# Optimization experiments

Measured on AMD Instinct MI355X. Metric: run time of the kernel, lower is better.

## Reference

```python
import jax, jax.numpy as jnp
import numpy as np

N, E, H, D_IN, L, G, T = 50000, 800000, 64, 64, 4, 128, 1

def _w(key, shape, fan_in):
    return jax.random.normal(key, shape, dtype=jnp.float32) / np.sqrt(fan_in)

def setup_inputs() -> dict:
    key = jax.random.key(0)
    ks = jax.random.split(key, 24)
    inp = {
        'x': jax.random.normal(ks[0], (N, D_IN), dtype=jnp.float32),
        'w': jax.random.normal(ks[1], (E, 1), dtype=jnp.float32),
        'src': jax.random.randint(ks[2], (E,), 0, N, dtype=jnp.int32),
        'dst': jax.random.randint(ks[3], (E,), 0, N, dtype=jnp.int32),
        'graph_id': jnp.sort(jax.random.randint(ks[4], (N,), 0, G, dtype=jnp.int32)),
        # input MLP (1 layer, last_activation None; SiLU applied in input_node_func)
        'W_in': _w(ks[5], (D_IN, H), D_IN), 'b_in': jnp.zeros((H,), jnp.float32),
        # per-layer message MLP: (2H+1 -> H -> H), SiLU mid and last
        'msg_W1': _w(ks[6], (L, 2 * H + 1, H), 2 * H + 1), 'msg_b1': jnp.zeros((L, H), jnp.float32),
        'msg_W2': _w(ks[7], (L, H, H), H), 'msg_b2': jnp.zeros((L, H), jnp.float32),
        # per-layer update MLP: (H -> H -> H), SiLU mid, last None
        'upd_W1': _w(ks[8], (L, H, H), H), 'upd_b1': jnp.zeros((L, H), jnp.float32),
        'upd_W2': _w(ks[9], (L, H, H), H), 'upd_b2': jnp.zeros((L, H), jnp.float32),
        # node-wise output MLP: (H -> H -> H), SiLU mid, last None
        'out_W1': _w(ks[10], (H, H), H), 'out_b1': jnp.zeros((H,), jnp.float32),
        'out_W2': _w(ks[11], (H, H), H), 'out_b2': jnp.zeros((H,), jnp.float32),
        # readout MLP: (3H -> H -> T), SiLU mid, last None
        'ro_W1': _w(ks[12], (3 * H, H), 3 * H), 'ro_b1': jnp.zeros((H,), jnp.float32),
        'ro_W2': _w(ks[13], (H, T), H), 'ro_b2': jnp.zeros((T,), jnp.float32),
    }
    return inp

def reference(x, w, src, dst, graph_id, W_in, b_in, msg_W1, msg_b1, msg_W2, msg_b2,
              upd_W1, upd_b1, upd_W2, upd_b2, out_W1, out_b1, out_W2, out_b2,
              ro_W1, ro_b1, ro_W2, ro_b2):
    silu = jax.nn.silu
    f = silu(x @ W_in + b_in)                                   # [N, H]
    sq = w * w                                                  # [E, 1]
    for l in range(L):
        mi = jnp.concatenate([f[src], f[dst], sq], axis=-1)     # [E, 2H+1]
        msg = silu(silu(mi @ msg_W1[l] + msg_b1[l]) @ msg_W2[l] + msg_b2[l])
        m = msg * jax.nn.sigmoid(msg)                           # gated message
        m_sum = jax.ops.segment_sum(m, dst, num_segments=N)     # scatter-sum to dst
        h_new = silu((m_sum + f) @ upd_W1[l] + upd_b1[l]) @ upd_W2[l] + upd_b2[l]
        f = h_new + f                                           # residual
    f = silu(f @ out_W1 + out_b1) @ out_W2 + out_b2             # node-wise output
    g_sum = jax.ops.segment_sum(f, graph_id, num_segments=G)
    cnt = jax.ops.segment_sum(jnp.ones((N, 1), f.dtype), graph_id, num_segments=G)
    g_mean = g_sum / jnp.maximum(cnt, 1.0)
    g_max = jax.ops.segment_max(f, graph_id, num_segments=G)
    readout = jnp.concatenate([g_sum, g_mean, g_max], axis=-1)  # [G, 3H]
    return silu(readout @ ro_W1 + ro_b1) @ ro_W2 + ro_b2        # [G, T]
```

## Files before the change

kernel.cpp:

```cpp
#include <hip/hip_runtime.h>

#define NN 50000
#define EE 800000
#define GG 128
#define LL 4
#define SCAN_B 196

typedef __bf16 bf16x8 __attribute__((ext_vector_type(8)));
typedef __bf16 bf16x4 __attribute__((ext_vector_type(4)));
typedef float  f32x4  __attribute__((ext_vector_type(4)));

__device__ __forceinline__ float silu_f(float x){
    float t = __builtin_amdgcn_exp2f(-1.44269504f * x);
    return x * __builtin_amdgcn_rcpf(1.0f + t);
}
__device__ __forceinline__ unsigned fenc(float v){
    unsigned u = __float_as_uint(v);
    return (u & 0x80000000u) ? ~u : (u | 0x80000000u);
}
__device__ __forceinline__ float fdec(unsigned u){
    return (u & 0x80000000u) ? __uint_as_float(u & 0x7fffffffu) : __uint_as_float(~u);
}

__global__ __launch_bounds__(256) void pack_k(
        const float* __restrict__ msgW1, const float* __restrict__ msgW2,
        const float* __restrict__ updW1, const float* __restrict__ updW2,
        const float* __restrict__ outW1, const float* __restrict__ outW2,
        const float* __restrict__ W_in, __bf16* __restrict__ pk){
    int m = blockIdx.x;
    const float* src;
    if(m<20){
        int l=m/5, r=m%5;
        if(r==0)      src = msgW1 + (size_t)l*129*64;
        else if(r==1) src = msgW1 + (size_t)l*129*64 + 64*64;
        else if(r==2) src = msgW2 + (size_t)l*64*64;
        else if(r==3) src = updW1 + (size_t)l*64*64;
        else          src = updW2 + (size_t)l*64*64;
    } else if(m==20) src=outW1; else if(m==21) src=outW2; else src=W_in;
    __bf16* dst = pk + (size_t)m*4096;
    int tid=threadIdx.x;
    #pragma unroll
    for(int i=0;i<16;++i){
        int idx = tid*16+i;
        int frag = idx>>9, lane=(idx>>3)&63, j=idx&7;
        int s=frag>>2, ng=frag&3, q=lane>>4, nn=lane&15;
        dst[idx] = (__bf16)src[(32*s+8*q+j)*64 + 16*ng + nn];
    }
}
__device__ __forceinline__ bf16x8 ldfrag(const __bf16* pk, int s, int ng, int lane){
    return *(const bf16x8*)&pk[(((s*4+ng)*64 + lane))*8];
}

__global__ __launch_bounds__(256) void input_mfma(const float* __restrict__ x,
        const __bf16* __restrict__ pkW, const float* __restrict__ bg,
        float* __restrict__ f, __bf16* __restrict__ f16, int N){
    int tid=threadIdx.x, wid=tid>>6, lane=tid&63;
    int q=lane>>4, nn=lane&15;
    bf16x8 Bf[2][4];
    #pragma unroll
    for(int s=0;s<2;++s)
        #pragma unroll
        for(int ng=0;ng<4;++ng) Bf[s][ng]=ldfrag(pkW,s,ng,lane);
    float bias[4];
    #pragma unroll
    for(int ng=0;ng<4;++ng) bias[ng]=bg[16*ng+nn];

    int ntiles=(N+15)/16;
    int gw=gridDim.x*4;
    for(int t=blockIdx.x*4+wid; t<ntiles; t+=gw){
        int m=t*16+nn; int mc=(m<N)?m:(N-1);
        float4 a0=*(const float4*)&x[(size_t)mc*64 + 8*q];
        float4 a1=*(const float4*)&x[(size_t)mc*64 + 8*q + 4];
        float4 a2=*(const float4*)&x[(size_t)mc*64 + 32 + 8*q];
        float4 a3=*(const float4*)&x[(size_t)mc*64 + 32 + 8*q + 4];
        bf16x8 af0, af1;
        af0[0]=(__bf16)a0.x; af0[1]=(__bf16)a0.y; af0[2]=(__bf16)a0.z; af0[3]=(__bf16)a0.w;
        af0[4]=(__bf16)a1.x; af0[5]=(__bf16)a1.y; af0[6]=(__bf16)a1.z; af0[7]=(__bf16)a1.w;
        af1[0]=(__bf16)a2.x; af1[1]=(__bf16)a2.y; af1[2]=(__bf16)a2.z; af1[3]=(__bf16)a2.w;
        af1[4]=(__bf16)a3.x; af1[5]=(__bf16)a3.y; af1[6]=(__bf16)a3.z; af1[7]=(__bf16)a3.w;
        #pragma unroll
        for(int ng=0;ng<4;++ng){
            f32x4 acc; acc[0]=bias[ng]; acc[1]=bias[ng]; acc[2]=bias[ng]; acc[3]=bias[ng];
            acc=__builtin_amdgcn_mfma_f32_16x16x32_bf16(af0,Bf[0][ng],acc,0,0,0);
            acc=__builtin_amdgcn_mfma_f32_16x16x32_bf16(af1,Bf[1][ng],acc,0,0,0);
            #pragma unroll
            for(int r=0;r<4;++r){
                int row=t*16+4*q+r;
                if(row<N){
                    float o=silu_f(acc[r]);
                    f[(size_t)row*64+16*ng+nn]=o;
                    f16[(size_t)row*64+16*ng+nn]=(__bf16)o;
                }
            }
        }
    }
}

__global__ void hist_k(const int* __restrict__ dst, int* __restrict__ deg, int E){
    int e=blockIdx.x*blockDim.x+threadIdx.x;
    if(e<E) atomicAdd(&deg[dst[e]],1);
}

__global__ __launch_bounds__(256) void scan1_k(const int* __restrict__ deg, int* __restrict__ curs,
        int* __restrict__ bsum, int N){
    __shared__ int sv[256];
    int tid=threadIdx.x;
    int idx=blockIdx.x*256+tid;
    int v=(idx<N)?deg[idx]:0;
    sv[tid]=v; __syncthreads();
    #pragma unroll
    for(int off=1; off<256; off<<=1){
        int a=(tid>=off)?sv[tid-off]:0;
        __syncthreads(); sv[tid]+=a; __syncthreads();
    }
    if(idx<N) curs[idx]=sv[tid]-v;
    if(tid==255) bsum[blockIdx.x]=sv[255];
}
__global__ __launch_bounds__(256) void scan2_k(int* __restrict__ bsum, int B){
    __shared__ int sv[256];
    int tid=threadIdx.x;
    int v=(tid<B)?bsum[tid]:0;
    sv[tid]=v; __syncthreads();
    #pragma unroll
    for(int off=1; off<256; off<<=1){
        int a=(tid>=off)?sv[tid-off]:0;
        __syncthreads(); sv[tid]+=a; __syncthreads();
    }
    if(tid<B) bsum[tid]=sv[tid]-v;
}
__global__ __launch_bounds__(256) void scan3_k(int* __restrict__ curs, const int* __restrict__ bsum, int N){
    int idx=blockIdx.x*256+threadIdx.x;
    if(idx<N) curs[idx]+=bsum[blockIdx.x];
}

__global__ void fill_k(const int* __restrict__ src, const int* __restrict__ dst,
                       const float* __restrict__ w, int* __restrict__ cursor,
                       int4* __restrict__ meta, int E){
    int e=blockIdx.x*blockDim.x+threadIdx.x;
    if(e<E){
        int d=dst[e];
        int r=atomicAdd(&cursor[d],1);
        float ww=w[e];
        int4 v; v.x=src[e]; v.y=d; v.z=__float_as_int(ww*ww); v.w=0;
        meta[r]=v;
    }
}

__global__ __launch_bounds__(256) void xy_mfma(const __bf16* __restrict__ f16,
        const __bf16* __restrict__ pkA, const __bf16* __restrict__ pkB,
        const float* __restrict__ b1, __bf16* __restrict__ XY,
        float* __restrict__ msum, int N){
    int tid=threadIdx.x, wid=tid>>6, lane=tid&63;
    int q=lane>>4, nn=lane&15;
    bf16x8 Bf[2][8];
    #pragma unroll
    for(int s=0;s<2;++s){
        #pragma unroll
        for(int ng=0;ng<4;++ng){ Bf[s][ng]=ldfrag(pkA,s,ng,lane); Bf[s][4+ng]=ldfrag(pkB,s,ng,lane); }
    }
    float bias[8];
    #pragma unroll
    for(int ng=0;ng<8;++ng) bias[ng]=(ng<4)?0.f:b1[16*(ng-4)+nn];
    int ntiles=(N+15)/16;
    int gw=gridDim.x*4;
    for(int t=blockIdx.x*4+wid; t<ntiles; t+=gw){
        int row=t*16+nn; if(row>=N) row=N-1;
        bf16x8 a0=*(const bf16x8*)&f16[(size_t)row*64 + 8*q];
        bf16x8 a1=*(const bf16x8*)&f16[(size_t)row*64 + 32 + 8*q];
        {
            float4 z; z.x=0.f; z.y=0.f; z.z=0.f; z.w=0.f;
            float4* mz=(float4*)(msum + (size_t)t*1024);
            int lim=(t*16+16<=N)?4:0;
            if(lim){
                #pragma unroll
                for(int i=0;i<4;++i) mz[i*64+lane]=z;
            } else {
                for(int rr=t*16; rr<N; ++rr) msum[(size_t)rr*64+lane]=0.f;
            }
        }
        #pragma unroll
        for(int ng=0;ng<8;++ng){
            f32x4 acc; acc[0]=bias[ng]; acc[1]=bias[ng]; acc[2]=bias[ng]; acc[3]=bias[ng];
            acc=__builtin_amdgcn_mfma_f32_16x16x32_bf16(a0,Bf[0][ng],acc,0,0,0);
            acc=__builtin_amdgcn_mfma_f32_16x16x32_bf16(a1,Bf[1][ng],acc,0,0,0);
            #pragma unroll
            for(int r=0;r<4;++r){
                int orow=t*16+4*q+r;
                if(orow<N) XY[(size_t)orow*128 + 16*ng + nn]=(__bf16)acc[r];
            }
        }
    }
}

__global__ __launch_bounds__(256) void edge_mfma4(
        const __bf16* __restrict__ XY, const int4* __restrict__ meta,
        const __bf16* __restrict__ pkW2,
        const float* __restrict__ W1, const float* __restrict__ b2,
        float* __restrict__ msum, int E){
    int tid=threadIdx.x, wid=tid>>6, lane=tid&63;
    int q=lane>>4, nn=lane&15;

    bf16x8 B2f[2][4];
    #pragma unroll
    for(int s=0;s<2;++s)
        #pragma unroll
        for(int ng=0;ng<4;++ng) B2f[s][ng]=ldfrag(pkW2,s,ng,lane);
    float w128lo[8], w128hi[8];
    #pragma unroll
    for(int j=0;j<8;++j){
        w128lo[j]=W1[128*64 + 8*q+j];
        w128hi[j]=W1[128*64 + 32+8*q+j];
    }
    float bias2[4];
    #pragma unroll
    for(int ng=0;ng<4;++ng) bias2[ng]=b2[16*ng+nn];

    __shared__ __align__(16) __bf16 sm16[4][32][68];
    int cpos = 4*(lane&15) + (lane>>4);

    int ntiles=E/32;
    int nw=gridDim.x*4;
    int chunk=(ntiles+nw-1)/nw;
    int wgl=blockIdx.x*4+wid;
    int t0=wgl*chunk, t1=t0+chunk; if(t1>ntiles) t1=ntiles;
    if(t0>=t1) return;

    int4 mv = meta[(size_t)t0*32 + (lane&31)];
    bf16x8 gx0lo,gx0hi,gy0lo,gy0hi,gx1lo,gx1hi,gy1lo,gy1hi;
    {
        int se0=__shfl(mv.x, nn,64),    de0=__shfl(mv.y, nn,64);
        int se1=__shfl(mv.x, 16+nn,64), de1=__shfl(mv.y, 16+nn,64);
        const __bf16* xp0=XY+(size_t)se0*128; const __bf16* yp0=XY+(size_t)de0*128+64;
        const __bf16* xp1=XY+(size_t)se1*128; const __bf16* yp1=XY+(size_t)de1*128+64;
        gx0lo=*(const bf16x8*)(xp0+8*q); gx0hi=*(const bf16x8*)(xp0+32+8*q);
        gy0lo=*(const bf16x8*)(yp0+8*q); gy0hi=*(const bf16x8*)(yp0+32+8*q);
        gx1lo=*(const bf16x8*)(xp1+8*q); gx1hi=*(const bf16x8*)(xp1+32+8*q);
        gy1lo=*(const bf16x8*)(yp1+8*q); gy1hi=*(const bf16x8*)(yp1+32+8*q);
    }
    int cur=__builtin_amdgcn_readlane(mv.y, 0);
    float vsum=0.f;

    for(int t=t0;t<t1;++t){
        bool hasn = (t+1<t1);
        int4 mvn = mv;
        if(hasn) mvn = meta[(size_t)(t+1)*32 + (lane&31)];

        int d_ = mv.y;
        float w2v = __int_as_float(mv.z);

        bf16x8 A0lo,A0hi,A1lo,A1hi;
        {
            float w2a = __shfl(w2v, nn, 64);
            float w2b = __shfl(w2v, 16+nn, 64);
            #pragma unroll
            for(int j=0;j<8;++j){
                A0lo[j]=(__bf16)silu_f((float)gx0lo[j] + (float)gy0lo[j] + w2a*w128lo[j]);
                A0hi[j]=(__bf16)silu_f((float)gx0hi[j] + (float)gy0hi[j] + w2a*w128hi[j]);
                A1lo[j]=(__bf16)silu_f((float)gx1lo[j] + (float)gy1lo[j] + w2b*w128lo[j]);
                A1hi[j]=(__bf16)silu_f((float)gx1hi[j] + (float)gy1hi[j] + w2b*w128hi[j]);
            }
        }
        if(hasn){
            int se0=__shfl(mvn.x, nn,64),    de0=__shfl(mvn.y, nn,64);
            int se1=__shfl(mvn.x, 16+nn,64), de1=__shfl(mvn.y, 16+nn,64);
            const __bf16* xp0=XY+(size_t)se0*128; const __bf16* yp0=XY+(size_t)de0*128+64;
            const __bf16* xp1=XY+(size_t)se1*128; const __bf16* yp1=XY+(size_t)de1*128+64;
            gx0lo=*(const bf16x8*)(xp0+8*q); gx0hi=*(const bf16x8*)(xp0+32+8*q);
            gy0lo=*(const bf16x8*)(yp0+8*q); gy0hi=*(const bf16x8*)(yp0+32+8*q);
            gx1lo=*(const bf16x8*)(xp1+8*q); gx1hi=*(const bf16x8*)(xp1+32+8*q);
            gy1lo=*(const bf16x8*)(yp1+8*q); gy1hi=*(const bf16x8*)(yp1+32+8*q);
        }
        #pragma unroll
        for(int h=0;h<2;++h){
            bf16x8 alo = h ? A1lo : A0lo;
            bf16x8 ahi = h ? A1hi : A0hi;
            f32x4 acc2[4];
            #pragma unroll
            for(int ng=0;ng<4;++ng){ f32x4 c; c[0]=bias2[ng]; c[1]=bias2[ng]; c[2]=bias2[ng]; c[3]=bias2[ng]; acc2[ng]=c; }
            #pragma unroll
            for(int ng=0;ng<4;++ng){
                acc2[ng]=__builtin_amdgcn_mfma_f32_16x16x32_bf16(alo,B2f[0][ng],acc2[ng],0,0,0);
                acc2[ng]=__builtin_amdgcn_mfma_f32_16x16x32_bf16(ahi,B2f[1][ng],acc2[ng],0,0,0);
            }
            #pragma unroll
            for(int r=0;r<4;++r){
                bf16x4 pv;
                #pragma unroll
                for(int ng=0;ng<4;++ng) pv[ng]=(__bf16)silu_f(silu_f(acc2[ng][r]));
                *(bf16x4*)&sm16[wid][16*h+4*q+r][4*nn] = pv;
            }
        }
        asm volatile("" ::: "memory");
        #pragma unroll
        for(int r=0;r<32;++r){
            int dr=__builtin_amdgcn_readlane(d_, r);
            if(dr!=cur){
                atomicAdd(&msum[(size_t)cur*64+lane], vsum);
                vsum=0.f; cur=dr;
            }
            vsum+=(float)sm16[wid][r][cpos];
        }
        asm volatile("" ::: "memory");
        mv = mvn;
    }
    atomicAdd(&msum[(size_t)cur*64+lane], vsum);
}

__global__ __launch_bounds__(256) void node_mfma(const float* __restrict__ A, const float* __restrict__ F,
        const __bf16* __restrict__ pkW1, const float* __restrict__ b1,
        const __bf16* __restrict__ pkW2, const float* __restrict__ b2,
        float* __restrict__ out, __bf16* __restrict__ out16, int N){
    int tid=threadIdx.x, wid=tid>>6, lane=tid&63;
    int q=lane>>4, nn=lane&15;

    bf16x8 B1f[2][4], B2f[2][4];
    #pragma unroll
    for(int s=0;s<2;++s)
        #pragma unroll
        for(int ng=0;ng<4;++ng){ B1f[s][ng]=ldfrag(pkW1,s,ng,lane); B2f[s][ng]=ldfrag(pkW2,s,ng,lane); }
    float bias1[4], bias2[4];
    #pragma unroll
    for(int ng=0;ng<4;++ng){ bias1[ng]=b1[16*ng+nn]; bias2[ng]=b2[16*ng+nn]; }

    __shared__ __align__(16) __bf16 sh1[4][16][72];
    __shared__ __align__(16) float sF[4][16][68];
    bool hasF = (F != nullptr);

    int ntiles=(N+15)/16;
    int gw=gridDim.x*4;
    for(int t=blockIdx.x*4+wid; t<ntiles; t+=gw){
        int m=t*16+nn;
        int mc=(m<N)?m:(N-1);
        float4 a0=*(const float4*)&A[(size_t)mc*64 + 8*q];
        float4 a1=*(const float4*)&A[(size_t)mc*64 + 8*q + 4];
        float4 a2=*(const float4*)&A[(size_t)mc*64 + 32 + 8*q];
        float4 a3=*(const float4*)&A[(size_t)mc*64 + 32 + 8*q + 4];
        if(hasF){
            float4 f0=*(const float4*)&F[(size_t)mc*64 + 8*q];
            float4 f1=*(const float4*)&F[(size_t)mc*64 + 8*q + 4];
            float4 f2_=*(const float4*)&F[(size_t)mc*64 + 32 + 8*q];
            float4 f3=*(const float4*)&F[(size_t)mc*64 + 32 + 8*q + 4];
            a0.x+=f0.x; a0.y+=f0.y; a0.z+=f0.z; a0.w+=f0.w;
            a1.x+=f1.x; a1.y+=f1.y; a1.z+=f1.z; a1.w+=f1.w;
            a2.x+=f2_.x; a2.y+=f2_.y; a2.z+=f2_.z; a2.w+=f2_.w;
            a3.x+=f3.x; a3.y+=f3.y; a3.z+=f3.z; a3.w+=f3.w;
            *(float4*)&sF[wid][nn][8*q]   = f0;
            *(float4*)&sF[wid][nn][8*q+4] = f1;
            *(float4*)&sF[wid][nn][32+8*q]   = f2_;
            *(float4*)&sF[wid][nn][32+8*q+4] = f3;
        }
        bf16x8 af0, af1;
        af0[0]=(__bf16)a0.x; af0[1]=(__bf16)a0.y; af0[2]=(__bf16)a0.z; af0[3]=(__bf16)a0.w;
        af0[4]=(__bf16)a1.x; af0[5]=(__bf16)a1.y; af0[6]=(__bf16)a1.z; af0[7]=(__bf16)a1.w;
        af1[0]=(__bf16)a2.x; af1[1]=(__bf16)a2.y; af1[2]=(__bf16)a2.z; af1[3]=(__bf16)a2.w;
        af1[4]=(__bf16)a3.x; af1[5]=(__bf16)a3.y; af1[6]=(__bf16)a3.z; af1[7]=(__bf16)a3.w;

        f32x4 acc[4];
        #pragma unroll
        for(int ng=0;ng<4;++ng){ f32x4 c; c[0]=bias1[ng]; c[1]=bias1[ng]; c[2]=bias1[ng]; c[3]=bias1[ng]; acc[ng]=c; }
        #pragma unroll
        for(int ng=0;ng<4;++ng){
            acc[ng]=__builtin_amdgcn_mfma_f32_16x16x32_bf16(af0,B1f[0][ng],acc[ng],0,0,0);
            acc[ng]=__builtin_amdgcn_mfma_f32_16x16x32_bf16(af1,B1f[1][ng],acc[ng],0,0,0);
        }
        #pragma unroll
        for(int ng=0;ng<4;++ng)
            #pragma unroll
            for(int r=0;r<4;++r)
                sh1[wid][4*q+r][16*ng+nn]=(__bf16)silu_f(acc[ng][r]);
        asm volatile("" ::: "memory");
        bf16x8 a20=*(const bf16x8*)&sh1[wid][nn][8*q];
        bf16x8 a21=*(const bf16x8*)&sh1[wid][nn][32+8*q];
        f32x4 acc2[4];
        #pragma unroll
        for(int ng=0;ng<4;++ng){ f32x4 c; c[0]=bias2[ng]; c[1]=bias2[ng]; c[2]=bias2[ng]; c[3]=bias2[ng]; acc2[ng]=c; }
        #pragma unroll
        for(int ng=0;ng<4;++ng){
            acc2[ng]=__builtin_amdgcn_mfma_f32_16x16x32_bf16(a20,B2f[0][ng],acc2[ng],0,0,0);
            acc2[ng]=__builtin_amdgcn_mfma_f32_16x16x32_bf16(a21,B2f[1][ng],acc2[ng],0,0,0);
        }
        #pragma unroll
        for(int ng=0;ng<4;++ng)
            #pragma unroll
            for(int r=0;r<4;++r){
                int row=t*16+4*q+r;
                if(row<N){
                    float o=acc2[ng][r];
                    if(hasF) o += sF[wid][4*q+r][16*ng+nn];
                    out[(size_t)row*64 + 16*ng + nn]=o;
                    if(out16) out16[(size_t)row*64 + 16*ng + nn]=(__bf16)o;
                }
            }
        asm volatile("" ::: "memory");
    }
}

__global__ __launch_bounds__(256) void seg_reduce_sorted(const float* __restrict__ f2, const int* __restrict__ gid,
        float* __restrict__ gsum, unsigned* __restrict__ gmaxu, float* __restrict__ cnt, int N){
    int wgl=blockIdx.x*4 + (threadIdx.x>>6);
    int lane=threadIdx.x&63;
    int W=gridDim.x*4;
    int chunk=(N+W-1)/W;
    int n0=wgl*chunk;
    int n1=n0+chunk; if(n1>N) n1=N;
    if(n0>=n1) return;
    int cur=gid[n0];
    float s=0.f, mx=-__builtin_inff(), c=0.f;
    for(int n=n0;n<n1;++n){
        int g=gid[n];
        float v=f2[(size_t)n*64+lane];
        if(g!=cur){
            atomicAdd(&gsum[(size_t)cur*64+lane], s);
            atomicMax(&gmaxu[(size_t)cur*64+lane], fenc(mx));
            if(lane==0) atomicAdd(&cnt[cur], c);
            s=0.f; mx=-__builtin_inff(); c=0.f; cur=g;
        }
        s+=v; mx=fmaxf(mx,v); c+=1.f;
    }
    atomicAdd(&gsum[(size_t)cur*64+lane], s);
    atomicMax(&gmaxu[(size_t)cur*64+lane], fenc(mx));
    if(lane==0) atomicAdd(&cnt[cur], c);
}

__global__ __launch_bounds__(256) void readout_k(const float* __restrict__ gsum, const unsigned* __restrict__ gmaxu,
        const float* __restrict__ cnt,
        const float* __restrict__ W1, const float* __restrict__ b1,
        const float* __restrict__ W2, const float* __restrict__ b2,
        float* __restrict__ out, int G){
    __shared__ __align__(16) float sr[4][192];
    int tid=threadIdx.x, wid=tid>>6, lane=tid&63;
    int g=blockIdx.x*4+wid;
    if(g<G){
        float s_=gsum[g*64+lane];
        float c=cnt[g];
        float mean=s_/fmaxf(c,1.0f);
        float mx=fdec(gmaxu[g*64+lane]);
        sr[wid][lane]=s_; sr[wid][64+lane]=mean; sr[wid][128+lane]=mx;
    }
    __syncthreads();
    if(g<G){
        float h=b1[lane];
        for(int k=0;k<192;k+=4){
            float4 r4=*(const float4*)&sr[wid][k];
            h += r4.x*W1[(k+0)*64+lane] + r4.y*W1[(k+1)*64+lane]
               + r4.z*W1[(k+2)*64+lane] + r4.w*W1[(k+3)*64+lane];
        }
        h=silu_f(h);
        float p=h*W2[lane];
        #pragma unroll
        for(int off=32;off>0;off>>=1) p += __shfl_down(p, off, 64);
        if(lane==0) out[g]=p+b2[0];
    }
}

extern "C" void kernel_launch(void* const* d_in, const int* in_sizes, int n_in,
                              void* d_out, int out_size, void* d_ws, size_t ws_size,
                              hipStream_t stream){
    const float* x     = (const float*)d_in[0];
    const float* w     = (const float*)d_in[1];
    const int*   src   = (const int*)d_in[2];
    const int*   dst   = (const int*)d_in[3];
    const int*   gid   = (const int*)d_in[4];
    const float* W_in  = (const float*)d_in[5];
    const float* b_in  = (const float*)d_in[6];
    const float* msgW1 = (const float*)d_in[7];
    const float* msgb1 = (const float*)d_in[8];
    const float* msgW2 = (const float*)d_in[9];
    const float* msgb2 = (const float*)d_in[10];
    const float* updW1 = (const float*)d_in[11];
    const float* updb1 = (const float*)d_in[12];
    const float* updW2 = (const float*)d_in[13];
    const float* updb2 = (const float*)d_in[14];
    const float* outW1 = (const float*)d_in[15];
    const float* outb1 = (const float*)d_in[16];
    const float* outW2 = (const float*)d_in[17];
    const float* outb2 = (const float*)d_in[18];
    const float* roW1  = (const float*)d_in[19];
    const float* rob1  = (const float*)d_in[20];
    const float* roW2  = (const float*)d_in[21];
    const float* rob2  = (const float*)d_in[22];

    float*  f     = (float*)d_ws;
    float*  msum  = f + (size_t)NN*64;
    float*  f2    = msum;
    __bf16* f16   = (__bf16*)(msum + (size_t)NN*64);
    __bf16* XY    = f16 + (size_t)NN*64;
    int4*   meta  = (int4*)(XY + (size_t)NN*128);
    __bf16* pk    = (__bf16*)(meta + EE);
    int*    deg   = (int*)(pk + 23*4096);
    int*    curs  = deg + 50048;
    int*    bsum  = curs + 50048;
    float*  gsum  = (float*)(bsum + 256);
    unsigned* gmaxu = (unsigned*)(gsum + GG*64);
    float*  cnt   = (float*)(gmaxu + GG*64);

    pack_k<<<dim3(23),dim3(256),0,stream>>>(msgW1, msgW2, updW1, updW2, outW1, outW2, W_in, pk);

    hipMemsetAsync(deg, 0, 50048*sizeof(int), stream);
    hist_k<<<dim3((EE+255)/256),dim3(256),0,stream>>>(dst, deg, EE);
    scan1_k<<<dim3(SCAN_B),dim3(256),0,stream>>>(deg, curs, bsum, NN);
    scan2_k<<<dim3(1),dim3(256),0,stream>>>(bsum, SCAN_B);
    scan3_k<<<dim3(SCAN_B),dim3(256),0,stream>>>(curs, bsum, NN);
    fill_k<<<dim3((EE+255)/256),dim3(256),0,stream>>>(src, dst, w, curs, meta, EE);

    input_mfma<<<dim3(782),dim3(256),0,stream>>>(x, pk + (size_t)22*4096, b_in, f, f16, NN);
    for(int l=0;l<LL;++l){
        xy_mfma<<<dim3(782),dim3(256),0,stream>>>(f16,
            pk + (size_t)(5*l+0)*4096, pk + (size_t)(5*l+1)*4096, msgb1 + l*64, XY, msum, NN);
        edge_mfma4<<<dim3(2048),dim3(256),0,stream>>>(XY, meta,
            pk + (size_t)(5*l+2)*4096,
            msgW1 + (size_t)l*129*64, msgb2 + l*64, msum, EE);
        node_mfma<<<dim3(782),dim3(256),0,stream>>>(msum, f,
            pk + (size_t)(5*l+3)*4096, updb1 + l*64,
            pk + (size_t)(5*l+4)*4096, updb2 + l*64, f, f16, NN);
    }
    node_mfma<<<dim3(782),dim3(256),0,stream>>>(f, nullptr,
        pk + (size_t)20*4096, outb1, pk + (size_t)21*4096, outb2, f2, nullptr, NN);
    hipMemsetAsync(gsum, 0, (size_t)(GG*64*2 + GG)*sizeof(float), stream);
    seg_reduce_sorted<<<dim3(256),dim3(256),0,stream>>>(f2, gid, gsum, gmaxu, cnt, NN);
    readout_k<<<dim3(32),dim3(256),0,stream>>>(gsum, gmaxu, cnt, roW1, rob1, roW2, rob2, (float*)d_out, GG);
}
```

Baseline: 593.8 us.

## Move msum zeroing into node kernel and ballot-based segment boundaries in edge kernel

The msum accumulator is no longer zeroed inside xy_mfma. It is memset once up front, and node_mfma now clears each row right after reading it, so the zeroing rides on a kernel that already touches that data. The edge kernel finds destination-change boundaries with a shuffle plus ballot instead of 32 scalar readlane comparisons. Grid sizes for xy_mfma and the edge kernel are also reduced. This removes a separate write pass over msum per layer but drops restrict on A, which may hurt load scheduling in node_mfma.

```diff
diff --git a/kernel.cpp b/kernel.cpp
--- a/kernel.cpp
+++ b/kernel.cpp
@@ -148,8 +148,7 @@
 
 __global__ __launch_bounds__(256) void xy_mfma(const __bf16* __restrict__ f16,
         const __bf16* __restrict__ pkA, const __bf16* __restrict__ pkB,
-        const float* __restrict__ b1, __bf16* __restrict__ XY,
-        float* __restrict__ msum, int N){
+        const float* __restrict__ b1, __bf16* __restrict__ XY, int N){
     int tid=threadIdx.x, wid=tid>>6, lane=tid&63;
     int q=lane>>4, nn=lane&15;
     bf16x8 Bf[2][8];
@@ -167,17 +166,6 @@
         int row=t*16+nn; if(row>=N) row=N-1;
         bf16x8 a0=*(const bf16x8*)&f16[(size_t)row*64 + 8*q];
         bf16x8 a1=*(const bf16x8*)&f16[(size_t)row*64 + 32 + 8*q];
-        {
-            float4 z; z.x=0.f; z.y=0.f; z.z=0.f; z.w=0.f;
-            float4* mz=(float4*)(msum + (size_t)t*1024);
-            int lim=(t*16+16<=N)?4:0;
-            if(lim){
-                #pragma unroll
-                for(int i=0;i<4;++i) mz[i*64+lane]=z;
-            } else {
-                for(int rr=t*16; rr<N; ++rr) msum[(size_t)rr*64+lane]=0.f;
-            }
-        }
         #pragma unroll
         for(int ng=0;ng<8;++ng){
             f32x4 acc; acc[0]=bias[ng]; acc[1]=bias[ng]; acc[2]=bias[ng]; acc[3]=bias[ng];
@@ -192,7 +180,7 @@
     }
 }
 
-__global__ __launch_bounds__(256) void edge_mfma4(
+__global__ __launch_bounds__(256) void edge_mfma5(
         const __bf16* __restrict__ XY, const int4* __restrict__ meta,
         const __bf16* __restrict__ pkW2,
         const float* __restrict__ W1, const float* __restrict__ b2,
@@ -291,14 +279,21 @@
             }
         }
         asm volatile("" ::: "memory");
-        #pragma unroll
-        for(int r=0;r<32;++r){
-            int dr=__builtin_amdgcn_readlane(d_, r);
-            if(dr!=cur){
-                atomicAdd(&msum[(size_t)cur*64+lane], vsum);
-                vsum=0.f; cur=dr;
-            }
-            vsum+=(float)sm16[wid][r][cpos];
+        {
+            int dprev = __shfl(d_, (lane+63)&63, 64);
+            unsigned long long bal = __ballot(lane>=1 && lane<32 && d_!=dprev);
+            unsigned bmask = (unsigned)bal;
+            int d0 = __builtin_amdgcn_readlane(d_, 0);
+            if(d0 != cur) bmask |= 1u;
+            #pragma unroll
+            for(int r=0;r<32;++r){
+                if(bmask & (1u<<r)){
+                    atomicAdd(&msum[(size_t)cur*64+lane], vsum);
+                    vsum=0.f;
+                    cur=__builtin_amdgcn_readlane(d_, r);
+                }
+                vsum += (float)sm16[wid][r][cpos];
+            }
         }
         asm volatile("" ::: "memory");
         mv = mvn;
@@ -306,10 +301,10 @@
     atomicAdd(&msum[(size_t)cur*64+lane], vsum);
 }
 
-__global__ __launch_bounds__(256) void node_mfma(const float* __restrict__ A, const float* __restrict__ F,
+__global__ __launch_bounds__(256) void node_mfma(float* A, const float* F,
         const __bf16* __restrict__ pkW1, const float* __restrict__ b1,
         const __bf16* __restrict__ pkW2, const float* __restrict__ b2,
-        float* __restrict__ out, __bf16* __restrict__ out16, int N){
+        float* __restrict__ out, __bf16* __restrict__ out16, int zeroA, int N){
     int tid=threadIdx.x, wid=tid>>6, lane=tid&63;
     int q=lane>>4, nn=lane&15;
 
@@ -348,6 +343,13 @@
             *(float4*)&sF[wid][nn][8*q+4] = f1;
             *(float4*)&sF[wid][nn][32+8*q]   = f2_;
             *(float4*)&sF[wid][nn][32+8*q+4] = f3;
+        }
+        if(zeroA && m<N){
+            float4 z; z.x=0.f; z.y=0.f; z.z=0.f; z.w=0.f;
+            *(float4*)&A[(size_t)mc*64 + 8*q]      = z;
+            *(float4*)&A[(size_t)mc*64 + 8*q + 4]  = z;
+            *(float4*)&A[(size_t)mc*64 + 32 + 8*q] = z;
+            *(float4*)&A[(size_t)mc*64 + 32 + 8*q + 4] = z;
         }
         bf16x8 af0, af1;
         af0[0]=(__bf16)a0.x; af0[1]=(__bf16)a0.y; af0[2]=(__bf16)a0.z; af0[3]=(__bf16)a0.w;
@@ -503,19 +505,20 @@
     scan3_k<<<dim3(SCAN_B),dim3(256),0,stream>>>(curs, bsum, NN);
     fill_k<<<dim3((EE+255)/256),dim3(256),0,stream>>>(src, dst, w, curs, meta, EE);
 
+    hipMemsetAsync(msum, 0, (size_t)NN*64*sizeof(float), stream);
     input_mfma<<<dim3(782),dim3(256),0,stream>>>(x, pk + (size_t)22*4096, b_in, f, f16, NN);
     for(int l=0;l<LL;++l){
-        xy_mfma<<<dim3(782),dim3(256),0,stream>>>(f16,
-            pk + (size_t)(5*l+0)*4096, pk + (size_t)(5*l+1)*4096, msgb1 + l*64, XY, msum, NN);
-        edge_mfma4<<<dim3(2048),dim3(256),0,stream>>>(XY, meta,
+        xy_mfma<<<dim3(512),dim3(256),0,stream>>>(f16,
+            pk + (size_t)(5*l+0)*4096, pk + (size_t)(5*l+1)*4096, msgb1 + l*64, XY, NN);
+        edge_mfma5<<<dim3(1280),dim3(256),0,stream>>>(XY, meta,
             pk + (size_t)(5*l+2)*4096,
             msgW1 + (size_t)l*129*64, msgb2 + l*64, msum, EE);
         node_mfma<<<dim3(782),dim3(256),0,stream>>>(msum, f,
             pk + (size_t)(5*l+3)*4096, updb1 + l*64,
-            pk + (size_t)(5*l+4)*4096, updb2 + l*64, f, f16, NN);
+            pk + (size_t)(5*l+4)*4096, updb2 + l*64, f, f16, 1, NN);
     }
     node_mfma<<<dim3(782),dim3(256),0,stream>>>(f, nullptr,
-        pk + (size_t)20*4096, outb1, pk + (size_t)21*4096, outb2, f2, nullptr, NN);
+        pk + (size_t)20*4096, outb1, pk + (size_t)21*4096, outb2, f2, nullptr, 0, NN);
     hipMemsetAsync(gsum, 0, (size_t)(GG*64*2 + GG)*sizeof(float), stream);
     seg_reduce_sorted<<<dim3(256),dim3(256),0,stream>>>(f2, gid, gsum, gmaxu, cnt, NN);
     readout_k<<<dim3(32),dim3(256),0,stream>>>(gsum, gmaxu, cnt, roW1, rob1, roW2, rob2, (float*)d_out, GG);
```

Result: faster. 573.1 us (-3.5%).
